# Kernel tuning notes

Hardware: AMD Instinct MI355X
Metric: run time of the kernel (lower is better)

## Reference

```python
import jax, jax.numpy as jnp
import numpy as np

B, L, D, C, H, NB = 2, 2048, 256, 8, 8, 2
S = 2                        # spatial coord dim of s
E = 2 * D - (C + 1)          # id-embedding width per D*2-(C+1)
FIN = 1 + S + E + C          # z + s + id-embed + conditionals
MAXLOC = 4096
DH = (2 * D) // H            # per-head dim


def _ln(x, sc, b):
    m = x.mean(-1, keepdims=True)
    v = ((x - m) ** 2).mean(-1, keepdims=True)
    return (x - m) * jax.lax.rsqrt(v + 1e-6) * sc + b


def setup_inputs() -> dict:
    key = jax.random.key(0)
    ks = iter(jax.random.split(key, 64))
    nrm = lambda shape: jax.random.normal(next(ks), shape, jnp.float32) * 0.02
    inp = {
        "z": jax.random.normal(next(ks), (B, L), jnp.float32),
        "conditionals": jax.random.normal(next(ks), (C,), jnp.float32),
        "s": jax.random.uniform(next(ks), (L, S), jnp.float32),
        "K": jax.random.uniform(next(ks), (L, L), jnp.float32),
        "embed": nrm((MAXLOC, E)),
        "W_in1": nrm((FIN, 4 * D)), "b_in1": jnp.zeros((4 * D,), jnp.float32),
        "W_in2": nrm((4 * D, D)), "b_in2": jnp.zeros((D,), jnp.float32),
        "bias_w": jnp.ones((NB,), jnp.float32), "bias_b": jnp.zeros((NB,), jnp.float32),
        "Wq": nrm((NB, D, 2 * D)), "bq": jnp.zeros((NB, 2 * D), jnp.float32),
        "Wk": nrm((NB, D, 2 * D)), "bk": jnp.zeros((NB, 2 * D), jnp.float32),
        "Wv": nrm((NB, D, 2 * D)), "bv": jnp.zeros((NB, 2 * D), jnp.float32),
        "Wo": nrm((NB, 2 * D, D)), "bo": jnp.zeros((NB, D), jnp.float32),
        "ln1_s": jnp.ones((NB, D), jnp.float32), "ln1_b": jnp.zeros((NB, D), jnp.float32),
        "ln2_s": jnp.ones((NB, D), jnp.float32), "ln2_b": jnp.zeros((NB, D), jnp.float32),
        "Wf1": nrm((NB, D, 4 * D)), "bf1": jnp.zeros((NB, 4 * D), jnp.float32),
        "Wf2": nrm((NB, 4 * D, D)), "bf2": jnp.zeros((NB, D), jnp.float32),
        "Wh1": nrm((D, 128)), "bh1": jnp.zeros((128,), jnp.float32),
        "Wh2": nrm((128, 1)), "bh2": jnp.zeros((1,), jnp.float32),
    }
    return inp


def reference(z, conditionals, s, K, embed, W_in1, b_in1, W_in2, b_in2,
              bias_w, bias_b, Wq, bq, Wk, bk, Wv, bv, Wo, bo,
              ln1_s, ln1_b, ln2_s, ln2_b, Wf1, bf1, Wf2, bf2,
              Wh1, bh1, Wh2, bh2):
    Bx, Lx = z.shape
    ids_e = embed[:Lx]  # ids = arange(L), so embedding lookup is a leading slice
    feats = jnp.concatenate([
        z[..., None],                                          # (B, L, 1)
        jnp.broadcast_to(s[None], (Bx, Lx, S)),                # (B, L, S)
        jnp.broadcast_to(ids_e[None], (Bx, Lx, E)),            # (B, L, E)
        jnp.broadcast_to(conditionals[None, None], (Bx, Lx, C)),  # cond_as_feats
    ], axis=-1)
    x = jax.nn.gelu(feats @ W_in1 + b_in1) @ W_in2 + b_in2     # (B, L, D)
    for i in range(NB):
        bias = bias_w[i] * K + bias_b[i]                        # learned scalar-affine kernel bias (L, L)
        h = _ln(x, ln1_s[i], ln1_b[i])
        q = (h @ Wq[i] + bq[i]).reshape(Bx, Lx, H, DH)
        k = (h @ Wk[i] + bk[i]).reshape(Bx, Lx, H, DH)
        v = (h @ Wv[i] + bv[i]).reshape(Bx, Lx, H, DH)
        scores = jnp.einsum('bqhd,bkhd->bhqk', q, k) / jnp.sqrt(jnp.float32(DH))
        scores = scores + bias[None, None]                      # broadcast over batch, heads
        a = jax.nn.softmax(scores, axis=-1)
        o = jnp.einsum('bhqk,bkhd->bqhd', a, v).reshape(Bx, Lx, 2 * D)
        x = x + (o @ Wo[i] + bo[i])
        h2 = _ln(x, ln2_s[i], ln2_b[i])
        x = x + jax.nn.gelu(h2 @ Wf1[i] + bf1[i]) @ Wf2[i] + bf2[i]
    return jax.nn.gelu(x @ Wh1 + bh1) @ Wh2 + bh2              # head MLP([128,1]) -> (B, L, 1)
```

## Files before the change

### kernel.cpp

```cpp
#include <hip/hip_runtime.h>
#include <math.h>

#define B_SZ 2
#define L_LEN 2048
#define D_MOD 256
#define H_HEADS 8
#define NB_BLK 2
#define S_SZ 2
#define E_SZ 503
#define C_SZ 8
#define FIN 514
#define FIN_PAD 576
#define LOG2E 1.44269504088896340736f
#define QSC (0.125f * LOG2E)

typedef short bf16x8 __attribute__((ext_vector_type(8)));
typedef float f32x4 __attribute__((ext_vector_type(4)));
typedef unsigned short u16x4 __attribute__((ext_vector_type(4)));
typedef unsigned short u16x8 __attribute__((ext_vector_type(8)));

#define OFF_IN1 0
#define OFF_IN2 589824
#define OFF_QKV 851968
#define OFF_O   1638400
#define OFF_F1  1900544
#define OFF_F2  2424832
#define OFF_H   2949120
#define WT_END  3047424

__device__ __forceinline__ unsigned short f2bf(float x) {
    unsigned u = __float_as_uint(x);
    u += 0x7FFFu + ((u >> 16) & 1u);
    return (unsigned short)(u >> 16);
}

__device__ __forceinline__ float bf2f(unsigned short h) {
    return __uint_as_float(((unsigned)h) << 16);
}

__device__ __forceinline__ float gelu_f(float x) {
    float x3 = x * x * x;
    return 0.5f * x * (1.0f + tanhf(0.7978845608028654f * (x + 0.044715f * x3)));
}

__device__ __forceinline__ void gll16(const void* g, void* l) {
    __builtin_amdgcn_global_load_lds(
        (const __attribute__((address_space(1))) unsigned int*)g,
        (__attribute__((address_space(3))) unsigned int*)l,
        16, 0, 0);
}

__global__ __launch_bounds__(256) void prep_kernel(
    const float* __restrict__ W_in1, const float* __restrict__ W_in2,
    const float* __restrict__ Wq, const float* __restrict__ Wk,
    const float* __restrict__ Wv, const float* __restrict__ Wo,
    const float* __restrict__ Wf1, const float* __restrict__ Wf2,
    const float* __restrict__ Wh1, const float* __restrict__ Kmat,
    const float* __restrict__ bias_w,
    const float* __restrict__ bq, const float* __restrict__ bk,
    const float* __restrict__ bv,
    const float* __restrict__ z, const float* __restrict__ s,
    const float* __restrict__ embed, const float* __restrict__ cond,
    unsigned short* __restrict__ wt, unsigned short* __restrict__ kmfrag,
    float* __restrict__ bqkv, unsigned short* __restrict__ feats)
{
    __shared__ unsigned short sT[64][65];
    int b = blockIdx.x;
    int t = threadIdx.x;

    if (b < 720) {
        const float* src; unsigned short* dst; int K, N, Kp, tile;
        float scale = 1.0f;
        if (b < 144)      { src = W_in1; dst = wt + OFF_IN1; K = 514;  N = 1024; Kp = 576;  tile = b; }
        else if (b < 208) { src = W_in2; dst = wt + OFF_IN2; K = 1024; N = 256;  Kp = 1024; tile = b - 144; }
        else if (b < 400) { int t2 = b - 208;
                            int sec = t2 >> 5; tile = t2 & 31;
                            int i = sec / 3, which = sec % 3;
                            const float* wsrc = which == 0 ? Wq : which == 1 ? Wk : Wv;
                            if (which == 0) scale = QSC;
                            src = wsrc + (size_t)i * 131072;
                            dst = wt + OFF_QKV + (size_t)i * 393216 + (size_t)which * 131072;
                            K = 256; N = 512; Kp = 256; }
        else if (b < 464) { int t2 = b - 400; int i = t2 >> 5; tile = t2 & 31;
                            src = Wo + (size_t)i * 131072; dst = wt + OFF_O + (size_t)i * 131072;
                            K = 512; N = 256; Kp = 512; }
        else if (b < 592) { int t2 = b - 464; int i = t2 >> 6; tile = t2 & 63;
                            src = Wf1 + (size_t)i * 262144; dst = wt + OFF_F1 + (size_t)i * 262144;
                            K = 256; N = 1024; Kp = 256; }
        else              { int t2 = b - 592; int i = t2 >> 6; tile = t2 & 63;
                            src = Wf2 + (size_t)i * 262144; dst = wt + OFF_F2 + (size_t)i * 262144;
                            K = 1024; N = 256; Kp = 1024; }

        int nt = N >> 6;
        int kt0 = (tile / nt) << 6;
        int nt0 = (tile % nt) << 6;
        #pragma unroll
        for (int p = 0; p < 4; p++) {
            int r = p * 16 + (t >> 4);
            int c = (t & 15) * 4;
            float4 v4 = make_float4(0.f, 0.f, 0.f, 0.f);
            if (kt0 + r < K) v4 = *(const float4*)(src + (size_t)(kt0 + r) * N + nt0 + c);
            sT[r][c + 0] = f2bf(v4.x * scale);
            sT[r][c + 1] = f2bf(v4.y * scale);
            sT[r][c + 2] = f2bf(v4.z * scale);
            sT[r][c + 3] = f2bf(v4.w * scale);
        }
        __syncthreads();
        int n = t >> 2, kq = (t & 3) * 16;
        u16x8 o0, o1;
        #pragma unroll
        for (int j = 0; j < 8; j++) {
            o0[j] = sT[kq + j][n];
            o1[j] = sT[kq + 8 + j][n];
        }
        unsigned short* dp = dst + (size_t)(nt0 + n) * Kp + kt0 + kq;
        *(u16x8*)(dp) = o0;
        *(u16x8*)(dp + 8) = o1;
    } else if (b < 1104) {
        int idx = (b - 720) * 256 + t;
        if (idx < 128 * 768) {
            int n = idx / 768, kk = idx % 768;
            int kz = kk & 255;
            float v = Wh1[(size_t)kz * 128 + n];
            unsigned short hi = f2bf(v);
            wt[OFF_H + idx] = (kk < 512) ? hi : f2bf(v - bf2f(hi));
        }
    } else if (b < 2128) {
        int tile = b - 1104;
        int kt = tile >> 5, qb = tile & 31;
        float s0 = bias_w[0] * LOG2E, s1 = bias_w[1] * LOG2E;
        int q0 = qb * 64 + ((t >> 6) << 4) + (((t >> 4) & 3) << 2);
        int k0 = kt * 64 + (t & 15);
        u16x8 a0, a1, b0, b1;
        #pragma unroll
        for (int c = 0; c < 4; c++)
            #pragma unroll
            for (int r = 0; r < 4; r++) {
                float v = Kmat[(size_t)(q0 + r) * L_LEN + k0 + c * 16];
                if (c < 2) { a0[c * 4 + r] = f2bf(v * s0); b0[c * 4 + r] = f2bf(v * s1); }
                else       { a1[(c - 2) * 4 + r] = f2bf(v * s0); b1[(c - 2) * 4 + r] = f2bf(v * s1); }
            }
        unsigned short* dp = kmfrag + (((size_t)(kt * 32 + qb)) * 256 + t) * 16;
        *(u16x8*)dp = a0;
        *(u16x8*)(dp + 8) = a1;
        unsigned short* dp1 = dp + ((size_t)1 << 22);
        *(u16x8*)dp1 = b0;
        *(u16x8*)(dp1 + 8) = b1;
    } else if (b < 2140) {
        int idx = (b - 2128) * 256 + t;
        if (idx < 2 * 1536) {
            int i = idx / 1536, c = idx % 1536;
            float v;
            if (c < 512)       v = bq[i * 512 + c] * QSC;
            else if (c < 1024) v = bk[i * 512 + c - 512];
            else               v = bv[i * 512 + c - 1024];
            bqkv[idx] = v;
        }
    } else {
        int idx = (b - 2140) * 256 + t;
        int l = idx / 144;
        int f0 = (idx % 144) * 4;
        u16x4 pk0, pk1;
        #pragma unroll
        for (int j = 0; j < 4; j++) {
            int f = f0 + j;
            float val;
            if (f >= 3 && f < 506)      val = embed[(size_t)l * E_SZ + (f - 3)];
            else if (f >= 1 && f < 3)   val = s[l * S_SZ + (f - 1)];
            else if (f >= 506 && f < FIN) val = cond[f - 506];
            else                        val = 0.0f;
            unsigned short hv = f2bf(val);
            pk0[j] = (f == 0) ? f2bf(z[l]) : hv;
            pk1[j] = (f == 0) ? f2bf(z[L_LEN + l]) : hv;
        }
        *(u16x4*)(feats + (size_t)l * FIN_PAD + f0) = pk0;
        *(u16x4*)(feats + (size_t)(L_LEN + l) * FIN_PAD + f0) = pk1;
    }
}

template<int ACT, int OMODE>
__global__ __launch_bounds__(256) void gemmW(
    const unsigned short* __restrict__ A, const unsigned short* __restrict__ Wt,
    const float* __restrict__ bias, unsigned short* __restrict__ Cb,
    unsigned short* __restrict__ Cbk, unsigned short* __restrict__ Cbv,
    int M, int N, int Kd, int lda)
{
    __shared__ unsigned short sA[2][64][64];
    __shared__ unsigned short sB[2][128][64];
    const int tid = threadIdx.x;
    const int l = tid & 63, w = tid >> 6;
    const int g = l >> 4, n16 = l & 15;
    const int wr = w >> 1, wc = w & 1;
    const int m0 = blockIdx.y * 64, n0 = blockIdx.x * 128;
    const int r8 = l >> 3;
    const int swz8 = ((l & 7) ^ r8) * 8;

    f32x4 acc[2][4];
    #pragma unroll
    for (int mi = 0; mi < 2; mi++)
        #pragma unroll
        for (int ni = 0; ni < 4; ni++)
            acc[mi][ni] = (f32x4){0.f, 0.f, 0.f, 0.f};

#define STAGEW(buf, k0)                                                         \
    do {                                                                        \
        _Pragma("unroll")                                                       \
        for (int p = 0; p < 2; p++) {                                           \
            int row = w * 16 + p * 8 + r8;                                      \
            gll16(A + (size_t)(m0 + row) * lda + (k0) + swz8,                   \
                  &sA[buf][w * 16 + p * 8][0]);                                 \
        }                                                                       \
        _Pragma("unroll")                                                       \
        for (int p = 0; p < 4; p++) {                                           \
            int row = w * 32 + p * 8 + r8;                                      \
            gll16(Wt + (size_t)(n0 + row) * Kd + (k0) + swz8,                   \
                  &sB[buf][w * 32 + p * 8][0]);                                 \
        }                                                                       \
    } while (0)

    STAGEW(0, 0);
    __syncthreads();

    int cur = 0;
    for (int k0 = 0; k0 < Kd; k0 += 64) {
        int nxt = cur ^ 1;
        if (k0 + 64 < Kd) STAGEW(nxt, k0 + 64);
        #pragma unroll
        for (int ks = 0; ks < 2; ks++) {
            bf16x8 af[2], bfr[4];
            #pragma unroll
            for (int mi = 0; mi < 2; mi++) {
                int row = wr * 32 + mi * 16 + n16;
                af[mi] = *(const bf16x8*)((const char*)&sA[cur][row][0]
                          + ((ks * 64 + g * 16) ^ ((n16 & 7) << 4)));
            }
            #pragma unroll
            for (int ni = 0; ni < 4; ni++) {
                int row = wc * 64 + ni * 16 + n16;
                bfr[ni] = *(const bf16x8*)((const char*)&sB[cur][row][0]
                          + ((ks * 64 + g * 16) ^ ((n16 & 7) << 4)));
            }
            #pragma unroll
            for (int mi = 0; mi < 2; mi++)
                #pragma unroll
                for (int ni = 0; ni < 4; ni++)
                    acc[mi][ni] = __builtin_amdgcn_mfma_f32_16x16x32_bf16(
                        af[mi], bfr[ni], acc[mi][ni], 0, 0, 0);
        }
        __syncthreads();
        cur = nxt;
    }
#undef STAGEW

    #pragma unroll
    for (int mi = 0; mi < 2; mi++) {
        #pragma unroll
        for (int ni = 0; ni < 4; ni++) {
            int col = n0 + wc * 64 + ni * 16 + n16;
            float bv = bias[col];
            #pragma unroll
            for (int r = 0; r < 4; r++) {
                int row = m0 + wr * 32 + mi * 16 + 4 * g + r;
                float val = acc[mi][ni][r] + bv;
                if (ACT == 1) val = gelu_f(val);
                if (OMODE == 1) {
                    Cb[(size_t)row * N + col] = f2bf(val);
                } else {
                    if (col < 1024) {
                        unsigned short* dst = (col < 512) ? Cb : Cbk;
                        dst[(size_t)row * 512 + (col & 511)] = f2bf(val);
                    } else {
                        Cbv[((size_t)(row >> 11) * 512 + (col - 1024)) * L_LEN + (row & (L_LEN - 1))] = f2bf(val);
                    }
                }
            }
        }
    }
}

template<int ACT, int OMODE, int BM>
__global__ __launch_bounds__(256) void gemm_bf16(
    const unsigned short* __restrict__ A, const unsigned short* __restrict__ Wt,
    const float* __restrict__ bias, float* __restrict__ Cf,
    unsigned short* __restrict__ Cb, int M, int N, int Kd, int lda)
{
    __shared__ unsigned short sA[2][BM][64];
    __shared__ unsigned short sB[2][64][64];
    const int tid = threadIdx.x;
    const int l = tid & 63, w = tid >> 6;
    const int g = l >> 4, n16 = l & 15;
    const int m0 = blockIdx.y * BM, n0 = blockIdx.x * 64;

    const int r8 = l >> 3;
    const int swz8 = ((l & 7) ^ r8) * 8;

    const int NMI = (BM == 64) ? 2 : 1;
    const int NNI = (BM == 16) ? 1 : 2;
    const int wr = w >> 1;
    const int wc = w & 1;

    f32x4 acc[2][2];
    #pragma unroll
    for (int mi = 0; mi < 2; mi++)
        #pragma unroll
        for (int ni = 0; ni < 2; ni++)
            acc[mi][ni] = (f32x4){0.f, 0.f, 0.f, 0.f};

#define STAGE(buf, k0)                                                          \
    do {                                                                        \
        if (BM == 64) {                                                         \
            _Pragma("unroll")                                                   \
            for (int p = 0; p < 2; p++) {                                       \
                int row = w * 16 + p * 8 + r8;                                  \
                gll16(A + (size_t)(m0 + row) * lda + (k0) + swz8,               \
                      &sA[buf][w * 16 + p * 8][0]);                             \
            }                                                                   \
        } else if (BM == 32) {                                                  \
            int row = w * 8 + r8;                                               \
            gll16(A + (size_t)(m0 + row) * lda + (k0) + swz8,                   \
                  &sA[buf][w * 8][0]);                                          \
        } else {                                                                \
            if (w < 2) {                                                        \
                int row = w * 8 + r8;                                           \
                gll16(A + (size_t)(m0 + row) * lda + (k0) + swz8,               \
                      &sA[buf][w * 8][0]);                                      \
            }                                                                   \
        }                                                                       \
        _Pragma("unroll")                                                       \
        for (int p = 0; p < 2; p++) {                                           \
            int row = w * 16 + p * 8 + r8;                                      \
            gll16(Wt + (size_t)(n0 + row) * Kd + (k0) + swz8,                   \
                  &sB[buf][w * 16 + p * 8][0]);                                 \
        }                                                                       \
    } while (0)

    STAGE(0, 0);
    __syncthreads();

    int cur = 0;
    for (int k0 = 0; k0 < Kd; k0 += 64) {
        int nxt = cur ^ 1;
        if (k0 + 64 < Kd) STAGE(nxt, k0 + 64);
        #pragma unroll
        for (int ks = 0; ks < 2; ks++) {
            bf16x8 af[2], bfr[2];
            #pragma unroll
            for (int mi = 0; mi < NMI; mi++) {
                int row = (BM == 64) ? (wr * 32 + mi * 16 + n16)
                        : (BM == 32) ? (wr * 16 + n16) : n16;
                af[mi] = *(const bf16x8*)((const char*)&sA[cur][row][0]
                          + ((ks * 64 + g * 16) ^ ((n16 & 7) << 4)));
            }
            #pragma unroll
            for (int ni = 0; ni < NNI; ni++) {
                int row = (BM == 16) ? (w * 16 + n16) : (wc * 32 + ni * 16 + n16);
                bfr[ni] = *(const bf16x8*)((const char*)&sB[cur][row][0]
                          + ((ks * 64 + g * 16) ^ ((n16 & 7) << 4)));
            }
            #pragma unroll
            for (int mi = 0; mi < NMI; mi++)
                #pragma unroll
                for (int ni = 0; ni < NNI; ni++)
                    acc[mi][ni] = __builtin_amdgcn_mfma_f32_16x16x32_bf16(
                        af[mi], bfr[ni], acc[mi][ni], 0, 0, 0);
        }
        __syncthreads();
        cur = nxt;
    }
#undef STAGE

    #pragma unroll
    for (int mi = 0; mi < NMI; mi++) {
        #pragma unroll
        for (int ni = 0; ni < NNI; ni++) {
            int col = (BM == 16) ? (n0 + w * 16 + n16)
                                 : (n0 + wc * 32 + ni * 16 + n16);
            float bv = bias[col];
            #pragma unroll
            for (int r = 0; r < 4; r++) {
                int row = (BM == 64) ? (m0 + wr * 32 + mi * 16 + 4 * g + r)
                        : (BM == 32) ? (m0 + wr * 16 + 4 * g + r)
                                     : (m0 + 4 * g + r);
                float val = acc[mi][ni][r] + bv;
                if (ACT == 1) val = gelu_f(val);
                if (OMODE == 0) {
                    Cf[(size_t)row * N + col] = val;
                } else if (OMODE == 1) {
                    Cb[(size_t)row * N + col] = f2bf(val);
                } else if (OMODE == 2) {
                    float* cp = Cf + (size_t)row * N + col;
                    *cp += val;
                } else if (OMODE == 5) {
                    float xnew = Cf[(size_t)row * N + col] + val;
                    unsigned short hi = f2bf(xnew);
                    unsigned short lo = f2bf(xnew - bf2f(hi));
                    unsigned short* orow = Cb + (size_t)row * 768;
                    orow[col] = hi;
                    orow[256 + col] = lo;
                    orow[512 + col] = hi;
                }
            }
        }
    }
}

__global__ __launch_bounds__(256) void ln_bf16(
    const float* __restrict__ x, const float* __restrict__ sc,
    const float* __restrict__ bi, unsigned short* __restrict__ out)
{
    int wave = threadIdx.x >> 6, lane = threadIdx.x & 63;
    int row = blockIdx.x * 4 + wave;
    const float* xr = x + (size_t)row * D_MOD;
    float4 v = *(const float4*)(xr + lane * 4);
    float s1 = v.x + v.y + v.z + v.w;
    float s2 = v.x * v.x + v.y * v.y + v.z * v.z + v.w * v.w;
    #pragma unroll
    for (int off = 1; off < 64; off <<= 1) {
        s1 += __shfl_xor(s1, off);
        s2 += __shfl_xor(s2, off);
    }
    float mean = s1 * (1.0f / 256.0f);
    float var = s2 * (1.0f / 256.0f) - mean * mean;
    float rs = rsqrtf(var + 1e-6f);
    float4 scv = *(const float4*)(sc + lane * 4);
    float4 bv  = *(const float4*)(bi + lane * 4);
    u16x4 o4;
    o4[0] = f2bf((v.x - mean) * rs * scv.x + bv.x);
    o4[1] = f2bf((v.y - mean) * rs * scv.y + bv.y);
    o4[2] = f2bf((v.z - mean) * rs * scv.z + bv.z);
    o4[3] = f2bf((v.w - mean) * rs * scv.w + bv.w);
    *(u16x4*)(out + (size_t)row * D_MOD + lane * 4) = o4;
}

__global__ __launch_bounds__(256, 2) void attn_mfma(
    const unsigned short* __restrict__ q, const unsigned short* __restrict__ k,
    const unsigned short* __restrict__ vt, const unsigned short* __restrict__ kmf,
    unsigned short* __restrict__ o)
{
    __shared__ unsigned short sK[2][64][64];
    __shared__ unsigned short sV[2][64][64];
    __shared__ unsigned short sP[4][16][72];

    const int tid = threadIdx.x;
    const int l = tid & 63, w = tid >> 6;
    const int g = l >> 4, n16 = l & 15;

    const int id = blockIdx.x;
    const int xcd = id & 7, rr2 = id >> 3;
    const int panel = xcd * 2 + (rr2 & 1);
    const int qi = rr2 >> 1;
    const int qblk = qi * 64, hh = panel & 7, b = panel >> 3;

    const int r8 = l >> 3;
    const int swz8 = ((l & 7) ^ r8) * 8;

    bf16x8 qf[2];
    {
        const unsigned short* qp = q + (size_t)(b * L_LEN + qblk + w * 16 + n16) * 512 + hh * 64;
        qf[0] = *(const bf16x8*)(qp + g * 8);
        qf[1] = *(const bf16x8*)(qp + 32 + g * 8);
    }
    bf16x8 onesf;
    #pragma unroll
    for (int j = 0; j < 8; j++) onesf[j] = (short)0x3F80;

    f32x4 o_acc[4];
    #pragma unroll
    for (int c = 0; c < 4; c++) o_acc[c] = (f32x4){0.f, 0.f, 0.f, 0.f};
    f32x4 l_acc = (f32x4){0.f, 0.f, 0.f, 0.f};

    const unsigned short* kbase = k + (size_t)b * L_LEN * 512 + hh * 64;
    const unsigned short* vbase = vt + ((size_t)b * 512 + hh * 64) * L_LEN;
    const unsigned short* kmbase = kmf + ((size_t)qi * 256 + tid) * 16;

    #pragma unroll
    for (int p = 0; p < 2; p++) {
        int row = w * 16 + p * 8 + r8;
        gll16(kbase + (size_t)row * 512 + swz8, &sK[0][w * 16 + p * 8][0]);
        gll16(vbase + (size_t)row * L_LEN + swz8, &sV[0][w * 16 + p * 8][0]);
    }
    u16x8 kmC0 = *(const u16x8*)kmbase;
    u16x8 kmC1 = *(const u16x8*)(kmbase + 8);
    __syncthreads();

    int cur = 0;
    for (int kt = 0; kt < L_LEN / 64; kt++) {
        const int nb = cur ^ 1;
        const int kblk2 = (kt + 1) << 6;
        u16x8 kmN0 = kmC0, kmN1 = kmC1;
        if (kt + 1 < L_LEN / 64) {
            #pragma unroll
            for (int p = 0; p < 2; p++) {
                int row = w * 16 + p * 8 + r8;
                gll16(kbase + (size_t)(kblk2 + row) * 512 + swz8, &sK[nb][w * 16 + p * 8][0]);
                gll16(vbase + (size_t)row * L_LEN + kblk2 + swz8, &sV[nb][w * 16 + p * 8][0]);
            }
            const unsigned short* kp2 = kmbase + (size_t)(kt + 1) * 131072;
            kmN0 = *(const u16x8*)kp2;
            kmN1 = *(const u16x8*)(kp2 + 8);
        }
        f32x4 sacc[4];
        #pragma unroll
        for (int c = 0; c < 4; c++)
            #pragma unroll
            for (int r = 0; r < 4; r++)
                sacc[c][r] = bf2f((unsigned short)(c < 2 ? kmC0[c * 4 + r] : kmC1[(c - 2) * 4 + r]));
        __builtin_amdgcn_s_setprio(1);
        #pragma unroll
        for (int ks = 0; ks < 2; ks++)
            #pragma unroll
            for (int c = 0; c < 4; c++) {
                int row = c * 16 + n16;
                bf16x8 kf = *(const bf16x8*)((const char*)&sK[cur][row][0]
                             + ((ks * 64 + g * 16) ^ ((n16 & 7) << 4)));
                sacc[c] = __builtin_amdgcn_mfma_f32_16x16x32_bf16(qf[ks], kf, sacc[c], 0, 0, 0);
            }
        __builtin_amdgcn_s_setprio(0);
        float p[4][4];
        #pragma unroll
        for (int r = 0; r < 4; r++)
            #pragma unroll
            for (int c = 0; c < 4; c++)
                p[r][c] = __builtin_amdgcn_exp2f(sacc[c][r]);
        #pragma unroll
        for (int r = 0; r < 4; r++)
            #pragma unroll
            for (int c = 0; c < 4; c++)
                sP[w][4 * g + r][c * 16 + n16] = f2bf(p[r][c]);
        __builtin_amdgcn_s_setprio(1);
        #pragma unroll
        for (int ks = 0; ks < 2; ks++) {
            bf16x8 pf = *(const bf16x8*)&sP[w][n16][ks * 32 + g * 8];
            l_acc = __builtin_amdgcn_mfma_f32_16x16x32_bf16(pf, onesf, l_acc, 0, 0, 0);
            #pragma unroll
            for (int c = 0; c < 4; c++) {
                int row = c * 16 + n16;
                bf16x8 vf = *(const bf16x8*)((const char*)&sV[cur][row][0]
                             + ((ks * 64 + g * 16) ^ ((n16 & 7) << 4)));
                o_acc[c] = __builtin_amdgcn_mfma_f32_16x16x32_bf16(pf, vf, o_acc[c], 0, 0, 0);
            }
        }
        __builtin_amdgcn_s_setprio(0);
        __syncthreads();
        cur = nb;
        kmC0 = kmN0;
        kmC1 = kmN1;
    }

    float inv[4];
    #pragma unroll
    for (int r = 0; r < 4; r++) inv[r] = 1.0f / l_acc[r];
    #pragma unroll
    for (int c = 0; c < 4; c++)
        #pragma unroll
        for (int r = 0; r < 4; r++)
            o[(size_t)(b * L_LEN + qblk + w * 16 + 4 * g + r) * 512 + hh * 64 + c * 16 + n16]
                = f2bf(o_acc[c][r] * inv[r]);
}

__global__ __launch_bounds__(256) void head_kernel(
    const unsigned short* __restrict__ A, const unsigned short* __restrict__ Wt,
    const float* __restrict__ bh1, const float* __restrict__ Wh2,
    const float* __restrict__ bh2, float* __restrict__ out)
{
    __shared__ unsigned short sA[2][16][64];
    __shared__ unsigned short sB[2][128][64];
    __shared__ float sRed[4][16];
    const int tid = threadIdx.x;
    const int l = tid & 63, w = tid >> 6;
    const int g = l >> 4, n16 = l & 15;
    const int m0 = blockIdx.x * 16;
    const int r8 = l >> 3;
    const int swz8 = ((l & 7) ^ r8) * 8;

    f32x4 acc[2];
    acc[0] = (f32x4){0.f, 0.f, 0.f, 0.f};
    acc[1] = (f32x4){0.f, 0.f, 0.f, 0.f};

#define HSTAGE(buf, k0)                                                         \
    do {                                                                        \
        if (w < 2) {                                                            \
            int row = w * 8 + r8;                                               \
            gll16(A + (size_t)(m0 + row) * 768 + (k0) + swz8,                   \
                  &sA[buf][w * 8][0]);                                          \
        }                                                                       \
        _Pragma("unroll")                                                       \
        for (int p = 0; p < 4; p++) {                                           \
            int row = w * 32 + p * 8 + r8;                                      \
            gll16(Wt + (size_t)row * 768 + (k0) + swz8,                         \
                  &sB[buf][w * 32 + p * 8][0]);                                 \
        }                                                                       \
    } while (0)

    HSTAGE(0, 0);
    __syncthreads();

    int cur = 0;
    for (int k0 = 0; k0 < 768; k0 += 64) {
        int nxt = cur ^ 1;
        if (k0 + 64 < 768) HSTAGE(nxt, k0 + 64);
        #pragma unroll
        for (int ks = 0; ks < 2; ks++) {
            bf16x8 af = *(const bf16x8*)((const char*)&sA[cur][n16][0]
                         + ((ks * 64 + g * 16) ^ ((n16 & 7) << 4)));
            #pragma unroll
            for (int ni = 0; ni < 2; ni++) {
                int row = w * 32 + ni * 16 + n16;
                bf16x8 bfr = *(const bf16x8*)((const char*)&sB[cur][row][0]
                              + ((ks * 64 + g * 16) ^ ((n16 & 7) << 4)));
                acc[ni] = __builtin_amdgcn_mfma_f32_16x16x32_bf16(af, bfr, acc[ni], 0, 0, 0);
            }
        }
        __syncthreads();
        cur = nxt;
    }
#undef HSTAGE

    float s[4];
    #pragma unroll
    for (int r = 0; r < 4; r++) {
        s[r] = 0.f;
        #pragma unroll
        for (int ni = 0; ni < 2; ni++) {
            int col = w * 32 + ni * 16 + n16;
            s[r] += gelu_f(acc[ni][r] + bh1[col]) * Wh2[col];
        }
        s[r] += __shfl_xor(s[r], 1);
        s[r] += __shfl_xor(s[r], 2);
        s[r] += __shfl_xor(s[r], 4);
        s[r] += __shfl_xor(s[r], 8);
    }
    if (n16 == 0) {
        #pragma unroll
        for (int r = 0; r < 4; r++) sRed[w][4 * g + r] = s[r];
    }
    __syncthreads();
    if (tid < 16)
        out[m0 + tid] = sRed[0][tid] + sRed[1][tid] + sRed[2][tid] + sRed[3][tid] + bh2[0];
}

extern "C" void kernel_launch(void* const* d_in, const int* in_sizes, int n_in,
                              void* d_out, int out_size, void* d_ws, size_t ws_size,
                              hipStream_t stream)
{
    const float* z      = (const float*)d_in[0];
    const float* cond   = (const float*)d_in[1];
    const float* s      = (const float*)d_in[2];
    const float* Kmat   = (const float*)d_in[3];
    const float* embed  = (const float*)d_in[4];
    const float* W_in1  = (const float*)d_in[5];
    const float* b_in1  = (const float*)d_in[6];
    const float* W_in2  = (const float*)d_in[7];
    const float* b_in2  = (const float*)d_in[8];
    const float* bias_w = (const float*)d_in[9];
    const float* bias_b = (const float*)d_in[10];
    const float* Wq     = (const float*)d_in[11];
    const float* bq     = (const float*)d_in[12];
    const float* Wk     = (const float*)d_in[13];
    const float* bk     = (const float*)d_in[14];
    const float* Wv     = (const float*)d_in[15];
    const float* bv     = (const float*)d_in[16];
    const float* Wo     = (const float*)d_in[17];
    const float* bo     = (const float*)d_in[18];
    const float* ln1_s  = (const float*)d_in[19];
    const float* ln1_b  = (const float*)d_in[20];
    const float* ln2_s  = (const float*)d_in[21];
    const float* ln2_b  = (const float*)d_in[22];
    const float* Wf1    = (const float*)d_in[23];
    const float* bf1    = (const float*)d_in[24];
    const float* Wf2    = (const float*)d_in[25];
    const float* bf2    = (const float*)d_in[26];
    const float* Wh1    = (const float*)d_in[27];
    const float* bh1    = (const float*)d_in[28];
    const float* Wh2    = (const float*)d_in[29];
    const float* bh2    = (const float*)d_in[30];
    float* out = (float*)d_out;
    (void)bias_b;

    const int M = B_SZ * L_LEN;
    char* base = (char*)d_ws;
    unsigned short* feats = (unsigned short*)base;
    float* x = (float*)(base + (size_t)M * FIN_PAD * 2);
    unsigned short* h    = (unsigned short*)((char*)x + (size_t)M * D_MOD * 4);
    unsigned short* hid1 = h    + (size_t)M * D_MOD;
    unsigned short* qb   = hid1 + (size_t)M * 1024;
    unsigned short* kb2  = qb   + (size_t)M * 512;
    unsigned short* vtb  = kb2  + (size_t)M * 512;
    unsigned short* ob   = vtb  + (size_t)M * 512;
    unsigned short* wt   = ob   + (size_t)M * 512;
    float* bqkv          = (float*)(wt + WT_END);
    unsigned short* kmfrag = (unsigned short*)(bqkv + 2 * 1536);

    prep_kernel<<<dim3(3292), dim3(256), 0, stream>>>(
        W_in1, W_in2, Wq, Wk, Wv, Wo, Wf1, Wf2, Wh1, Kmat, bias_w,
        bq, bk, bv, z, s, embed, cond, wt, kmfrag, bqkv, feats);

    gemmW<1, 1><<<dim3(8, 64), 256, 0, stream>>>(feats, wt + OFF_IN1, b_in1, hid1, nullptr, nullptr, M, 1024, FIN_PAD, FIN_PAD);
    gemm_bf16<0, 0, 16><<<dim3(4, 256), 256, 0, stream>>>(hid1, wt + OFF_IN2, b_in2, x, nullptr, M, 256, 1024, 1024);

    for (int i = 0; i < NB_BLK; i++) {
        ln_bf16<<<dim3(M / 4), 256, 0, stream>>>(x, ln1_s + i * D_MOD, ln1_b + i * D_MOD, h);
        gemmW<0, 4><<<dim3(12, 64), 256, 0, stream>>>(h, wt + OFF_QKV + (size_t)i * 393216, bqkv + i * 1536, qb, kb2, vtb, M, 1536, 256, 256);
        attn_mfma<<<dim3(512), 256, 0, stream>>>(qb, kb2, vtb, kmfrag + ((size_t)i << 22), ob);
        gemm_bf16<0, 2, 16><<<dim3(4, 256), 256, 0, stream>>>(ob, wt + OFF_O + (size_t)i * 131072, bo + i * D_MOD, x, nullptr, M, 256, 512, 512);
        ln_bf16<<<dim3(M / 4), 256, 0, stream>>>(x, ln2_s + i * D_MOD, ln2_b + i * D_MOD, h);
        gemmW<1, 1><<<dim3(8, 64), 256, 0, stream>>>(h, wt + OFF_F1 + (size_t)i * 262144, bf1 + i * 1024, hid1, nullptr, nullptr, M, 1024, 256, 256);
        if (i == 0)
            gemm_bf16<0, 2, 16><<<dim3(4, 256), 256, 0, stream>>>(hid1, wt + OFF_F2 + (size_t)i * 262144, bf2 + i * D_MOD, x, nullptr, M, 256, 1024, 1024);
        else
            gemm_bf16<0, 5, 16><<<dim3(4, 256), 256, 0, stream>>>(hid1, wt + OFF_F2 + (size_t)i * 262144, bf2 + i * D_MOD, x, qb, M, 256, 1024, 1024);
    }
    head_kernel<<<dim3(256), 256, 0, stream>>>(qb, wt + OFF_H, bh1, Wh2, bh2, out);
}
```

Baseline: 234.3 us.

## Stage transposed bias tiles via LDS and triple-buffer K/V in attention

The precomputed kernel-bias matrix is now stored as a plain transposed bf16 matrix, built through an LDS transpose in the prep kernel for coalesced reads, instead of per-thread fragments. The attention kernel loads bias tiles asynchronously into LDS alongside K and V. K/V move from double to triple buffering with prefetch two tiles ahead, using explicit vmcnt waits and a single barrier per iteration in place of the trailing syncthreads. This aims to hide global load latency and cut synchronisation, at the cost of more LDS per block, which may reduce occupancy.

```diff
diff --git a/kernel.cpp b/kernel.cpp
--- a/kernel.cpp
+++ b/kernel.cpp
@@ -61,14 +61,15 @@
     const float* __restrict__ bv,
     const float* __restrict__ z, const float* __restrict__ s,
     const float* __restrict__ embed, const float* __restrict__ cond,
-    unsigned short* __restrict__ wt, unsigned short* __restrict__ kmfrag,
+    unsigned short* __restrict__ wt, unsigned short* __restrict__ kbt,
     float* __restrict__ bqkv, unsigned short* __restrict__ feats)
 {
-    __shared__ unsigned short sT[64][65];
+    __shared__ float sTf[64][65];
     int b = blockIdx.x;
     int t = threadIdx.x;
 
     if (b < 720) {
+        unsigned short (*sT)[65] = (unsigned short (*)[65])&sTf[0][0];
         const float* src; unsigned short* dst; int K, N, Kp, tile;
         float scale = 1.0f;
         if (b < 144)      { src = W_in1; dst = wt + OFF_IN1; K = 514;  N = 1024; Kp = 576;  tile = b; }
@@ -127,25 +128,32 @@
         }
     } else if (b < 2128) {
         int tile = b - 1104;
-        int kt = tile >> 5, qb = tile & 31;
+        int qt0 = (tile & 31) << 6, kt0 = (tile >> 5) << 6;
+        int rr = t >> 4, cc = (t & 15) << 2;
+        #pragma unroll
+        for (int p = 0; p < 4; p++) {
+            int qr = p * 16 + rr;
+            float4 v4 = *(const float4*)(Kmat + (size_t)(qt0 + qr) * L_LEN + kt0 + cc);
+            sTf[cc + 0][qr] = v4.x;
+            sTf[cc + 1][qr] = v4.y;
+            sTf[cc + 2][qr] = v4.z;
+            sTf[cc + 3][qr] = v4.w;
+        }
+        __syncthreads();
         float s0 = bias_w[0] * LOG2E, s1 = bias_w[1] * LOG2E;
-        int q0 = qb * 64 + ((t >> 6) << 4) + (((t >> 4) & 3) << 2);
-        int k0 = kt * 64 + (t & 15);
+        int kr = t >> 2, qc = (t & 3) << 4;
         u16x8 a0, a1, b0, b1;
         #pragma unroll
-        for (int c = 0; c < 4; c++)
-            #pragma unroll
-            for (int r = 0; r < 4; r++) {
-                float v = Kmat[(size_t)(q0 + r) * L_LEN + k0 + c * 16];
-                if (c < 2) { a0[c * 4 + r] = f2bf(v * s0); b0[c * 4 + r] = f2bf(v * s1); }
-                else       { a1[(c - 2) * 4 + r] = f2bf(v * s0); b1[(c - 2) * 4 + r] = f2bf(v * s1); }
-            }
-        unsigned short* dp = kmfrag + (((size_t)(kt * 32 + qb)) * 256 + t) * 16;
-        *(u16x8*)dp = a0;
-        *(u16x8*)(dp + 8) = a1;
-        unsigned short* dp1 = dp + ((size_t)1 << 22);
-        *(u16x8*)dp1 = b0;
-        *(u16x8*)(dp1 + 8) = b1;
+        for (int j = 0; j < 8; j++) {
+            float v = sTf[kr][qc + j];
+            a0[j] = f2bf(v * s0); b0[j] = f2bf(v * s1);
+            float v2 = sTf[kr][qc + 8 + j];
+            a1[j] = f2bf(v2 * s0); b1[j] = f2bf(v2 * s1);
+        }
+        unsigned short* d0 = kbt + (size_t)(kt0 + kr) * L_LEN + qt0 + qc;
+        *(u16x8*)d0 = a0; *(u16x8*)(d0 + 8) = a1;
+        unsigned short* d1 = d0 + (size_t)L_LEN * L_LEN;
+        *(u16x8*)d1 = b0; *(u16x8*)(d1 + 8) = b1;
     } else if (b < 2140) {
         int idx = (b - 2128) * 256 + t;
         if (idx < 2 * 1536) {
@@ -434,11 +442,12 @@
 
 __global__ __launch_bounds__(256, 2) void attn_mfma(
     const unsigned short* __restrict__ q, const unsigned short* __restrict__ k,
-    const unsigned short* __restrict__ vt, const unsigned short* __restrict__ kmf,
+    const unsigned short* __restrict__ vt, const unsigned short* __restrict__ kmt,
     unsigned short* __restrict__ o)
 {
-    __shared__ unsigned short sK[2][64][64];
-    __shared__ unsigned short sV[2][64][64];
+    __shared__ unsigned short sK[3][64][64];
+    __shared__ unsigned short sV[3][64][64];
+    __shared__ unsigned short sKmT[2][64][64];
     __shared__ unsigned short sP[4][16][72];
 
     const int tid = threadIdx.x;
@@ -471,40 +480,55 @@
 
     const unsigned short* kbase = k + (size_t)b * L_LEN * 512 + hh * 64;
     const unsigned short* vbase = vt + ((size_t)b * 512 + hh * 64) * L_LEN;
-    const unsigned short* kmbase = kmf + ((size_t)qi * 256 + tid) * 16;
-
-    #pragma unroll
-    for (int p = 0; p < 2; p++) {
-        int row = w * 16 + p * 8 + r8;
-        gll16(kbase + (size_t)row * 512 + swz8, &sK[0][w * 16 + p * 8][0]);
-        gll16(vbase + (size_t)row * L_LEN + swz8, &sV[0][w * 16 + p * 8][0]);
-    }
-    u16x8 kmC0 = *(const u16x8*)kmbase;
-    u16x8 kmC1 = *(const u16x8*)(kmbase + 8);
-    __syncthreads();
+
+    const int krow = w * 16 + r8;
+    const int krow2 = w * 16 + 8 + r8;
+
+    gll16(kmt + (size_t)krow * L_LEN + qblk + swz8, &sKmT[0][w * 16][0]);
+    gll16(kmt + (size_t)krow2 * L_LEN + qblk + swz8, &sKmT[0][w * 16 + 8][0]);
+    gll16(kbase + (size_t)krow * 512 + swz8, &sK[0][w * 16][0]);
+    gll16(kbase + (size_t)krow2 * 512 + swz8, &sK[0][w * 16 + 8][0]);
+    gll16(vbase + (size_t)krow * L_LEN + swz8, &sV[0][w * 16][0]);
+    gll16(vbase + (size_t)krow2 * L_LEN + swz8, &sV[0][w * 16 + 8][0]);
+    gll16(kbase + (size_t)(64 + krow) * 512 + swz8, &sK[1][w * 16][0]);
+    gll16(kbase + (size_t)(64 + krow2) * 512 + swz8, &sK[1][w * 16 + 8][0]);
+    gll16(vbase + (size_t)krow * L_LEN + 64 + swz8, &sV[1][w * 16][0]);
+    gll16(vbase + (size_t)krow2 * L_LEN + 64 + swz8, &sV[1][w * 16 + 8][0]);
 
     int cur = 0;
     for (int kt = 0; kt < L_LEN / 64; kt++) {
-        const int nb = cur ^ 1;
-        const int kblk2 = (kt + 1) << 6;
-        u16x8 kmN0 = kmC0, kmN1 = kmC1;
+        if (kt < L_LEN / 64 - 1) {
+            asm volatile("s_waitcnt vmcnt(4)" ::: "memory");
+        } else {
+            asm volatile("s_waitcnt vmcnt(0)" ::: "memory");
+        }
+        __builtin_amdgcn_s_barrier();
+        __builtin_amdgcn_sched_barrier(0);
+
         if (kt + 1 < L_LEN / 64) {
-            #pragma unroll
-            for (int p = 0; p < 2; p++) {
-                int row = w * 16 + p * 8 + r8;
-                gll16(kbase + (size_t)(kblk2 + row) * 512 + swz8, &sK[nb][w * 16 + p * 8][0]);
-                gll16(vbase + (size_t)row * L_LEN + kblk2 + swz8, &sV[nb][w * 16 + p * 8][0]);
-            }
-            const unsigned short* kp2 = kmbase + (size_t)(kt + 1) * 131072;
-            kmN0 = *(const u16x8*)kp2;
-            kmN1 = *(const u16x8*)(kp2 + 8);
-        }
+            const int kb1 = (kt + 1) << 6;
+            int kmb = (kt + 1) & 1;
+            gll16(kmt + (size_t)(kb1 + krow) * L_LEN + qblk + swz8, &sKmT[kmb][w * 16][0]);
+            gll16(kmt + (size_t)(kb1 + krow2) * L_LEN + qblk + swz8, &sKmT[kmb][w * 16 + 8][0]);
+        }
+        if (kt + 2 < L_LEN / 64) {
+            const int kb2 = (kt + 2) << 6;
+            int wbuf = cur + 2; if (wbuf >= 3) wbuf -= 3;
+            gll16(kbase + (size_t)(kb2 + krow) * 512 + swz8, &sK[wbuf][w * 16][0]);
+            gll16(kbase + (size_t)(kb2 + krow2) * 512 + swz8, &sK[wbuf][w * 16 + 8][0]);
+            gll16(vbase + (size_t)krow * L_LEN + kb2 + swz8, &sV[wbuf][w * 16][0]);
+            gll16(vbase + (size_t)krow2 * L_LEN + kb2 + swz8, &sV[wbuf][w * 16 + 8][0]);
+        }
+
         f32x4 sacc[4];
         #pragma unroll
-        for (int c = 0; c < 4; c++)
+        for (int c = 0; c < 4; c++) {
+            const char* kb_ = (const char*)&sKmT[kt & 1][c * 16 + n16][0];
+            u16x4 kmv = *(const u16x4*)(kb_ + ((32 * w + 8 * g) ^ ((n16 & 7) << 4)));
             #pragma unroll
             for (int r = 0; r < 4; r++)
-                sacc[c][r] = bf2f((unsigned short)(c < 2 ? kmC0[c * 4 + r] : kmC1[(c - 2) * 4 + r]));
+                sacc[c][r] = bf2f((unsigned short)kmv[r]);
+        }
         __builtin_amdgcn_s_setprio(1);
         #pragma unroll
         for (int ks = 0; ks < 2; ks++)
@@ -541,10 +565,8 @@
             }
         }
         __builtin_amdgcn_s_setprio(0);
-        __syncthreads();
-        cur = nb;
-        kmC0 = kmN0;
-        kmC1 = kmN1;
+
+        cur = cur + 1; if (cur >= 3) cur -= 3;
     }
 
     float inv[4];
@@ -689,11 +711,11 @@
     unsigned short* ob   = vtb  + (size_t)M * 512;
     unsigned short* wt   = ob   + (size_t)M * 512;
     float* bqkv          = (float*)(wt + WT_END);
-    unsigned short* kmfrag = (unsigned short*)(bqkv + 2 * 1536);
+    unsigned short* kbt  = (unsigned short*)(bqkv + 2 * 1536);
 
     prep_kernel<<<dim3(3292), dim3(256), 0, stream>>>(
         W_in1, W_in2, Wq, Wk, Wv, Wo, Wf1, Wf2, Wh1, Kmat, bias_w,
-        bq, bk, bv, z, s, embed, cond, wt, kmfrag, bqkv, feats);
+        bq, bk, bv, z, s, embed, cond, wt, kbt, bqkv, feats);
 
     gemmW<1, 1><<<dim3(8, 64), 256, 0, stream>>>(feats, wt + OFF_IN1, b_in1, hid1, nullptr, nullptr, M, 1024, FIN_PAD, FIN_PAD);
     gemm_bf16<0, 0, 16><<<dim3(4, 256), 256, 0, stream>>>(hid1, wt + OFF_IN2, b_in2, x, nullptr, M, 256, 1024, 1024);
@@ -701,7 +723,7 @@
     for (int i = 0; i < NB_BLK; i++) {
         ln_bf16<<<dim3(M / 4), 256, 0, stream>>>(x, ln1_s + i * D_MOD, ln1_b + i * D_MOD, h);
         gemmW<0, 4><<<dim3(12, 64), 256, 0, stream>>>(h, wt + OFF_QKV + (size_t)i * 393216, bqkv + i * 1536, qb, kb2, vtb, M, 1536, 256, 256);
-        attn_mfma<<<dim3(512), 256, 0, stream>>>(qb, kb2, vtb, kmfrag + ((size_t)i << 22), ob);
+        attn_mfma<<<dim3(512), 256, 0, stream>>>(qb, kb2, vtb, kbt + (size_t)i * L_LEN * L_LEN, ob);
         gemm_bf16<0, 2, 16><<<dim3(4, 256), 256, 0, stream>>>(ob, wt + OFF_O + (size_t)i * 131072, bo + i * D_MOD, x, nullptr, M, 256, 512, 512);
         ln_bf16<<<dim3(M / 4), 256, 0, stream>>>(x, ln2_s + i * D_MOD, ln2_b + i * D_MOD, h);
         gemmW<1, 1><<<dim3(8, 64), 256, 0, stream>>>(h, wt + OFF_F1 + (size_t)i * 262144, bf1 + i * 1024, hid1, nullptr, nullptr, M, 1024, 256, 256);
```

After: 237.3 us. Within noise of the previous version (+1.3%).

## Split attention over two KV halves with a separate combine kernel

Applied to the files above, without the earlier changes.

The attention kernel now splits the key/value sequence into two halves, doubling the grid to 1024 blocks. Each block writes an unnormalized partial output in bf16 plus its row sums, and a new combine kernel adds the two halves and normalizes. This targets low occupancy and the long serial KV loop, raising launch bounds to 4 blocks per CU. The P tile in shared memory also gets an XOR swizzle in place of padding. The cost is an extra kernel launch, more global traffic for the partials, and extra bf16 rounding of the partial outputs.

```diff
diff --git a/kernel.cpp b/kernel.cpp
--- a/kernel.cpp
+++ b/kernel.cpp
@@ -432,24 +432,27 @@
     *(u16x4*)(out + (size_t)row * D_MOD + lane * 4) = o4;
 }
 
-__global__ __launch_bounds__(256, 2) void attn_mfma(
+__global__ __launch_bounds__(256, 4) void attn_mfma(
     const unsigned short* __restrict__ q, const unsigned short* __restrict__ k,
     const unsigned short* __restrict__ vt, const unsigned short* __restrict__ kmf,
-    unsigned short* __restrict__ o)
+    unsigned short* __restrict__ po, float* __restrict__ pl)
 {
     __shared__ unsigned short sK[2][64][64];
     __shared__ unsigned short sV[2][64][64];
-    __shared__ unsigned short sP[4][16][72];
+    __shared__ unsigned short sP[4][16][64];
 
     const int tid = threadIdx.x;
     const int l = tid & 63, w = tid >> 6;
     const int g = l >> 4, n16 = l & 15;
 
     const int id = blockIdx.x;
-    const int xcd = id & 7, rr2 = id >> 3;
-    const int panel = xcd * 2 + (rr2 & 1);
-    const int qi = rr2 >> 1;
+    const int xcd = id & 7, rest = id >> 3;
+    const int panel = xcd * 2 + (rest & 1);
+    const int sub = rest >> 1;
+    const int half = sub & 1;
+    const int qi = sub >> 1;
     const int qblk = qi * 64, hh = panel & 7, b = panel >> 3;
+    const int kv0 = half * 1024;
 
     const int r8 = l >> 3;
     const int swz8 = ((l & 7) ^ r8) * 8;
@@ -469,9 +472,10 @@
     for (int c = 0; c < 4; c++) o_acc[c] = (f32x4){0.f, 0.f, 0.f, 0.f};
     f32x4 l_acc = (f32x4){0.f, 0.f, 0.f, 0.f};
 
-    const unsigned short* kbase = k + (size_t)b * L_LEN * 512 + hh * 64;
-    const unsigned short* vbase = vt + ((size_t)b * 512 + hh * 64) * L_LEN;
-    const unsigned short* kmbase = kmf + ((size_t)qi * 256 + tid) * 16;
+    const unsigned short* kbase = k + ((size_t)(b * L_LEN) + kv0) * 512 + hh * 64;
+    const unsigned short* vbase = vt + ((size_t)b * 512 + hh * 64) * L_LEN + kv0;
+    const unsigned short* kmbase = kmf + (((size_t)qi * 256 + tid) * 16)
+                                 + (size_t)(half * 16) * 131072;
 
     #pragma unroll
     for (int p = 0; p < 2; p++) {
@@ -484,11 +488,11 @@
     __syncthreads();
 
     int cur = 0;
-    for (int kt = 0; kt < L_LEN / 64; kt++) {
+    for (int kt = 0; kt < 16; kt++) {
         const int nb = cur ^ 1;
         const int kblk2 = (kt + 1) << 6;
         u16x8 kmN0 = kmC0, kmN1 = kmC1;
-        if (kt + 1 < L_LEN / 64) {
+        if (kt + 1 < 16) {
             #pragma unroll
             for (int p = 0; p < 2; p++) {
                 int row = w * 16 + p * 8 + r8;
@@ -523,14 +527,17 @@
             for (int c = 0; c < 4; c++)
                 p[r][c] = __builtin_amdgcn_exp2f(sacc[c][r]);
         #pragma unroll
-        for (int r = 0; r < 4; r++)
+        for (int r = 0; r < 4; r++) {
+            int prow = 4 * g + r;
             #pragma unroll
             for (int c = 0; c < 4; c++)
-                sP[w][4 * g + r][c * 16 + n16] = f2bf(p[r][c]);
+                sP[w][prow][(c * 16 + n16) ^ ((prow & 7) << 3)] = f2bf(p[r][c]);
+        }
         __builtin_amdgcn_s_setprio(1);
         #pragma unroll
         for (int ks = 0; ks < 2; ks++) {
-            bf16x8 pf = *(const bf16x8*)&sP[w][n16][ks * 32 + g * 8];
+            bf16x8 pf = *(const bf16x8*)((const char*)&sP[w][n16][0]
+                         + (((ks * 32 + g * 8) ^ ((n16 & 7) << 3)) * 2));
             l_acc = __builtin_amdgcn_mfma_f32_16x16x32_bf16(pf, onesf, l_acc, 0, 0, 0);
             #pragma unroll
             for (int c = 0; c < 4; c++) {
@@ -547,15 +554,37 @@
         kmC1 = kmN1;
     }
 
-    float inv[4];
-    #pragma unroll
-    for (int r = 0; r < 4; r++) inv[r] = 1.0f / l_acc[r];
+    unsigned short* pob = po + (size_t)half * (4096 * 512);
     #pragma unroll
     for (int c = 0; c < 4; c++)
         #pragma unroll
         for (int r = 0; r < 4; r++)
-            o[(size_t)(b * L_LEN + qblk + w * 16 + 4 * g + r) * 512 + hh * 64 + c * 16 + n16]
-                = f2bf(o_acc[c][r] * inv[r]);
+            pob[(size_t)(b * L_LEN + qblk + w * 16 + 4 * g + r) * 512 + hh * 64 + c * 16 + n16]
+                = f2bf(o_acc[c][r]);
+    if (n16 == 0) {
+        #pragma unroll
+        for (int r = 0; r < 4; r++)
+            pl[(size_t)half * 32768 + (size_t)(b * L_LEN + qblk + w * 16 + 4 * g + r) * 8 + hh]
+                = l_acc[r];
+    }
+}
+
+__global__ __launch_bounds__(256) void attn_combine(
+    const unsigned short* __restrict__ po, const float* __restrict__ pl,
+    unsigned short* __restrict__ ob)
+{
+    int idx = (blockIdx.x * 256 + threadIdx.x) * 8;
+    int row = idx >> 9, hh = (idx & 511) >> 6;
+    u16x8 a = *(const u16x8*)(po + idx);
+    u16x8 b8 = *(const u16x8*)(po + (size_t)(4096 * 512) + idx);
+    float l0 = pl[(size_t)row * 8 + hh];
+    float l1 = pl[32768 + (size_t)row * 8 + hh];
+    float inv = 1.0f / (l0 + l1);
+    u16x8 o;
+    #pragma unroll
+    for (int j = 0; j < 8; j++)
+        o[j] = f2bf((bf2f((unsigned short)a[j]) + bf2f((unsigned short)b8[j])) * inv);
+    *(u16x8*)(ob + idx) = o;
 }
 
 __global__ __launch_bounds__(256) void head_kernel(
@@ -690,6 +719,8 @@
     unsigned short* wt   = ob   + (size_t)M * 512;
     float* bqkv          = (float*)(wt + WT_END);
     unsigned short* kmfrag = (unsigned short*)(bqkv + 2 * 1536);
+    unsigned short* po   = kmfrag + ((size_t)2 << 22);
+    float* pl            = (float*)(po + (size_t)2 * 4096 * 512);
 
     prep_kernel<<<dim3(3292), dim3(256), 0, stream>>>(
         W_in1, W_in2, Wq, Wk, Wv, Wo, Wf1, Wf2, Wh1, Kmat, bias_w,
@@ -701,7 +732,8 @@
     for (int i = 0; i < NB_BLK; i++) {
         ln_bf16<<<dim3(M / 4), 256, 0, stream>>>(x, ln1_s + i * D_MOD, ln1_b + i * D_MOD, h);
         gemmW<0, 4><<<dim3(12, 64), 256, 0, stream>>>(h, wt + OFF_QKV + (size_t)i * 393216, bqkv + i * 1536, qb, kb2, vtb, M, 1536, 256, 256);
-        attn_mfma<<<dim3(512), 256, 0, stream>>>(qb, kb2, vtb, kmfrag + ((size_t)i << 22), ob);
+        attn_mfma<<<dim3(1024), 256, 0, stream>>>(qb, kb2, vtb, kmfrag + ((size_t)i << 22), po, pl);
+        attn_combine<<<dim3(1024), 256, 0, stream>>>(po, pl, ob);
         gemm_bf16<0, 2, 16><<<dim3(4, 256), 256, 0, stream>>>(ob, wt + OFF_O + (size_t)i * 131072, bo + i * D_MOD, x, nullptr, M, 256, 512, 512);
         ln_bf16<<<dim3(M / 4), 256, 0, stream>>>(x, ln2_s + i * D_MOD, ln2_b + i * D_MOD, h);
         gemmW<1, 1><<<dim3(8, 64), 256, 0, stream>>>(h, wt + OFF_F1 + (size_t)i * 262144, bf1 + i * 1024, hid1, nullptr, nullptr, M, 1024, 256, 256);
```

New measurement: 222.8 us (median of 3 runs). 4.9% less time.
